# Performance work log

Hardware: AMD Instinct MI355X
Metric: run time of the kernel (lower is better)

## Reference

```python
import jax, jax.numpy as jnp
import numpy as np

HEADS = 8
DIM_HEAD = 64
QUERY_DIM = 512
CONTEXT_DIM = 512
OUT_DIM = 512
INNER = HEADS * DIM_HEAD  # 512


def setup_inputs() -> dict:
    key = jax.random.key(0)
    ks = jax.random.split(key, 6)
    B, N, S, M = 2, 1024, 4, 2048
    x = jax.random.normal(ks[0], (B, N, S, QUERY_DIM), dtype=jnp.float32)
    context = jax.random.normal(ks[1], (B, M, CONTEXT_DIM), dtype=jnp.float32)
    # Linear weights stored as [in, out] so y = x @ W (matches torch Linear with W.T)
    Wq = jax.random.normal(ks[2], (QUERY_DIM, INNER), dtype=jnp.float32) / np.sqrt(QUERY_DIM)
    Wkv = jax.random.normal(ks[3], (CONTEXT_DIM, 2 * INNER), dtype=jnp.float32) / np.sqrt(CONTEXT_DIM)
    Wo = jax.random.normal(ks[4], (INNER, OUT_DIM), dtype=jnp.float32) / np.sqrt(INNER)
    bo = jax.random.normal(ks[5], (OUT_DIM,), dtype=jnp.float32) * 0.01
    return {"x": x, "context": context, "Wq": Wq, "Wkv": Wkv, "Wo": Wo, "bo": bo}


def reference(x, context, Wq, Wkv, Wo, bo):
    B, N, S, _ = x.shape
    M = context.shape[1]
    scale = DIM_HEAD ** -0.5
    # projections
    q = (x @ Wq).reshape(B, N, S, HEADS, DIM_HEAD)            # b n s h d
    kv = context @ Wkv                                        # b m (2*inner)
    k, v = jnp.split(kv, 2, axis=-1)
    k = k.reshape(B, M, HEADS, DIM_HEAD)                      # b m h d
    v = v.reshape(B, M, HEADS, DIM_HEAD)
    # attention scores: [(b h) s n m] expressed as bhsnm
    sim = jnp.einsum('bnshd,bmhd->bhsnm', q, k) * scale
    attn = jax.nn.softmax(sim, axis=-1)
    out = jnp.einsum('bhsnm,bmhd->bnshd', attn, v)            # b n s h d
    out = out.reshape(B, N, S, INNER)
    return out @ Wo + bo
```

## Files before the change

kernel.cpp:

```cpp
#include <hip/hip_runtime.h>

typedef __bf16 bf16;
typedef __bf16 bf16x8 __attribute__((ext_vector_type(8)));
typedef __bf16 bf16x4 __attribute__((ext_vector_type(4)));
typedef float f32x4 __attribute__((ext_vector_type(4)));

#define SCL 0.18033688011112042f

#define GLOAD_LDS16(g, l)                                          \
  __builtin_amdgcn_global_load_lds(                                \
      (const __attribute__((address_space(1))) void*)(g),          \
      (__attribute__((address_space(3))) void*)(l), 16, 0, 0)

__global__ __launch_bounds__(256) void prep_kernel(const float* __restrict__ x,
                                                   const float* __restrict__ ctx,
                                                   const float* __restrict__ Wq,
                                                   const float* __restrict__ Wkv,
                                                   const float* __restrict__ Wo,
                                                   bf16* __restrict__ xb,
                                                   bf16* __restrict__ cb,
                                                   bf16* __restrict__ Wqt,
                                                   bf16* __restrict__ Wkvt,
                                                   bf16* __restrict__ Wot) {
  const int bid = blockIdx.x;
  const int tid = threadIdx.x;
  if (bid < 3072) {
    const float* src;
    bf16* dst;
    size_t off;
    if (bid < 2048) { src = x; dst = xb; off = (size_t)bid * 2048; }
    else            { src = ctx; dst = cb; off = (size_t)(bid - 2048) * 2048; }
    size_t i = off + (size_t)tid * 8;
    float4 a0 = *(const float4*)&src[i];
    float4 a1 = *(const float4*)&src[i + 4];
    bf16x8 o;
    o[0] = (bf16)a0.x; o[1] = (bf16)a0.y; o[2] = (bf16)a0.z; o[3] = (bf16)a0.w;
    o[4] = (bf16)a1.x; o[5] = (bf16)a1.y; o[6] = (bf16)a1.z; o[7] = (bf16)a1.w;
    *(bf16x8*)&dst[i] = o;
  } else {
    __shared__ float tile[32][33];
    const int idx = bid - 3072;
    const int bx = idx & 63;
    const int k0 = (idx >> 6) * 32;
    const float* W; bf16* Wt; int N, n0;
    if (bx < 16)      { W = Wq;  Wt = Wqt;  N = 512;  n0 = bx * 32; }
    else if (bx < 48) { W = Wkv; Wt = Wkvt; N = 1024; n0 = (bx - 16) * 32; }
    else              { W = Wo;  Wt = Wot;  N = 512;  n0 = (bx - 48) * 32; }
    const int j = tid & 31, i0 = tid >> 5;
#pragma unroll
    for (int ii = 0; ii < 4; ii++) {
      int i = i0 * 4 + ii;
      tile[i][j] = W[(size_t)(k0 + i) * N + n0 + j];
    }
    __syncthreads();
#pragma unroll
    for (int ii = 0; ii < 4; ii++) {
      int i = i0 * 4 + ii;
      Wt[(size_t)(n0 + i) * 512 + k0 + j] = (bf16)tile[j][i];
    }
  }
}

__device__ __forceinline__ void gemm128x64_core(const bf16* __restrict__ A,
                                                const bf16* __restrict__ Bt,
                                                int m0, int n0,
                                                bf16* As, bf16* Bs,
                                                f32x4 (&acc)[4][2],
                                                int wave, int lane) {
  const int l15 = lane & 15, quad = lane >> 4;
  const int psw = l15 & 7;
  const int lrow = lane >> 3;
  const int gchunk = (lane & 7) ^ lrow;
  const bf16* Ag = A + (size_t)(m0 + wave * 32 + lrow) * 512 + gchunk * 8;
  const bf16* Bg = Bt + (size_t)(n0 + wave * 16 + lrow) * 512 + gchunk * 8;
  bf16* Asw = As + wave * 32 * 64;
  bf16* Bsw = Bs + wave * 16 * 64;
  const int wm = (wave >> 1) * 64, wn = (wave & 1) * 32;

  for (int kt = 0; kt < 512; kt += 64) {
#pragma unroll
    for (int g = 0; g < 4; g++)
      GLOAD_LDS16(Ag + kt + (size_t)(g * 8) * 512, Asw + g * 8 * 64);
#pragma unroll
    for (int g = 0; g < 2; g++)
      GLOAD_LDS16(Bg + kt + (size_t)(g * 8) * 512, Bsw + g * 8 * 64);
    __syncthreads();
#pragma unroll
    for (int h = 0; h < 2; h++) {
      bf16x8 af[4], bfr[2];
#pragma unroll
      for (int i = 0; i < 4; i++)
        af[i] = *(const bf16x8*)&As[(wm + i * 16 + l15) * 64 + (((h * 4 + quad) ^ psw) * 8)];
#pragma unroll
      for (int j = 0; j < 2; j++)
        bfr[j] = *(const bf16x8*)&Bs[(wn + j * 16 + l15) * 64 + (((h * 4 + quad) ^ psw) * 8)];
#pragma unroll
      for (int i = 0; i < 4; i++)
#pragma unroll
        for (int j = 0; j < 2; j++)
          acc[i][j] = __builtin_amdgcn_mfma_f32_16x16x32_bf16(af[i], bfr[j], acc[i][j], 0, 0, 0);
    }
    __syncthreads();
  }
}

__global__ __launch_bounds__(256) void proj_kernel(const bf16* __restrict__ xb,
                                                   const bf16* __restrict__ cb,
                                                   const bf16* __restrict__ Wqt,
                                                   const bf16* __restrict__ Wkvt,
                                                   bf16* __restrict__ qb,
                                                   bf16* __restrict__ Kb,
                                                   bf16* __restrict__ Vtb) {
  __shared__ __align__(16) bf16 As[128 * 64];
  __shared__ __align__(16) bf16 Bs[64 * 64];
  const int tid = threadIdx.x;
  const int wave = tid >> 6, lane = tid & 63;
  const int quad = lane >> 4, l15 = lane & 15;
  const int bid = blockIdx.x;
  f32x4 acc[4][2] = {};
  const int wm = (wave >> 1) * 64, wn = (wave & 1) * 32;

  if (bid < 512) {
    const int m0 = (bid >> 3) * 128, n0 = (bid & 7) * 64;
    gemm128x64_core(xb, Wqt, m0, n0, As, Bs, acc, wave, lane);
#pragma unroll
    for (int i = 0; i < 4; i++) {
      const int rowb = m0 + wm + i * 16 + quad * 4;
#pragma unroll
      for (int j = 0; j < 2; j++) {
        const int col = n0 + wn + j * 16 + l15;
#pragma unroll
        for (int r = 0; r < 4; r++)
          qb[(size_t)(rowb + r) * 512 + col] = (bf16)(acc[i][j][r] * SCL);
      }
    }
  } else {
    const int idx = bid - 512;
    const int m0 = (idx >> 4) * 128, n0 = (idx & 15) * 64;
    gemm128x64_core(cb, Wkvt, m0, n0, As, Bs, acc, wave, lane);
#pragma unroll
    for (int i = 0; i < 4; i++) {
      const int rowb = m0 + wm + i * 16 + quad * 4;
#pragma unroll
      for (int j = 0; j < 2; j++) {
        const int col = n0 + wn + j * 16 + l15;
        if (col < 512) {
#pragma unroll
          for (int r = 0; r < 4; r++)
            Kb[(size_t)(rowb + r) * 512 + col] = (bf16)acc[i][j][r];
        } else {
          const int hh = (col - 512) >> 6, d = (col - 512) & 63;
          const int bb = rowb >> 11, mb = rowb & 2047;
          bf16x4 pk;
          pk[0] = (bf16)acc[i][j][0]; pk[1] = (bf16)acc[i][j][1];
          pk[2] = (bf16)acc[i][j][2]; pk[3] = (bf16)acc[i][j][3];
          *(bf16x4*)&Vtb[((size_t)(bb * 8 + hh) * 64 + d) * 2048 + mb] = pk;
        }
      }
    }
  }
}

__global__ __launch_bounds__(256) void outproj_kernel(const bf16* __restrict__ attn,
                                                      const bf16* __restrict__ Wot,
                                                      float* __restrict__ out,
                                                      const float* __restrict__ bias) {
  __shared__ __align__(16) bf16 As[128 * 64];
  __shared__ __align__(16) bf16 Bs[64 * 64];
  const int tid = threadIdx.x;
  const int wave = tid >> 6, lane = tid & 63;
  const int quad = lane >> 4, l15 = lane & 15;
  const int bid = blockIdx.x;
  const int m0 = (bid >> 3) * 128, n0 = (bid & 7) * 64;
  f32x4 acc[4][2] = {};
  gemm128x64_core(attn, Wot, m0, n0, As, Bs, acc, wave, lane);
  const int wm = (wave >> 1) * 64, wn = (wave & 1) * 32;
#pragma unroll
  for (int i = 0; i < 4; i++) {
    const int rowb = m0 + wm + i * 16 + quad * 4;
#pragma unroll
    for (int j = 0; j < 2; j++) {
      const int col = n0 + wn + j * 16 + l15;
      const float bv = bias[col];
#pragma unroll
      for (int r = 0; r < 4; r++)
        out[(size_t)(rowb + r) * 512 + col] = acc[i][j][r] + bv;
    }
  }
}

__global__ __launch_bounds__(256, 2) void attn_kernel(const bf16* __restrict__ q,
                                                      const bf16* __restrict__ Kb,
                                                      const bf16* __restrict__ Vtb,
                                                      bf16* __restrict__ attn_out) {
  const int tid = threadIdx.x;
  const int wave = tid >> 6, lane = tid & 63;
  const int quad = lane >> 4, l15 = lane & 15;
  const int bid = blockIdx.x;
  const int nt = bid & 7, h = (bid >> 3) & 7, s = (bid >> 6) & 3, b = bid >> 8;
  const int n0 = nt * 128;

  __shared__ __align__(16) bf16 Kl[2][64 * 64];
  __shared__ __align__(16) bf16 Vl[2][64 * 64];
  __shared__ __align__(16) bf16 Pl[4][32 * 64];
  bf16* Pw = &Pl[wave][0];

  size_t qoff[2];
  bf16x8 qf[2][2];
#pragma unroll
  for (int cg = 0; cg < 2; cg++) {
    const int n = n0 + wave * 32 + cg * 16 + l15;
    qoff[cg] = ((size_t)((b * 1024 + n) * 4 + s)) * 512 + h * 64;
    qf[cg][0] = *(const bf16x8*)&q[qoff[cg] + quad * 8];
    qf[cg][1] = *(const bf16x8*)&q[qoff[cg] + 32 + quad * 8];
  }

  f32x4 o[2][4] = {};
  f32x4 ol[2] = {};
  bf16x8 ones;
#pragma unroll
  for (int i = 0; i < 8; i++) ones[i] = (bf16)1.0f;

  const int srow = tid >> 2, c0 = tid & 3;
  const bf16* Kg = Kb + (size_t)(b * 2048 + srow) * 512 + h * 64 + c0 * 16;
  const bf16* Vg = Vtb + ((size_t)(b * 8 + h) * 64 + srow) * 2048 + c0 * 16;
  const int ssw = srow & 7;
  const int koff0 = srow * 64 + ((c0 * 2) ^ ssw) * 8;
  const int koff1 = srow * 64 + ((c0 * 2 + 1) ^ ssw) * 8;

  uint4 kr0 = *(const uint4*)Kg;
  uint4 kr1 = *(const uint4*)(Kg + 8);
  uint4 vr0 = *(const uint4*)Vg;
  uint4 vr1 = *(const uint4*)(Vg + 8);
  *(uint4*)&Kl[0][koff0] = kr0; *(uint4*)&Kl[0][koff1] = kr1;
  *(uint4*)&Vl[0][koff0] = vr0; *(uint4*)&Vl[0][koff1] = vr1;

  const int psw = l15 & 7;

  for (int t = 0; t < 32; ++t) {
    __syncthreads();
    if (t < 31) {
      const bf16* kg = Kg + (size_t)(t + 1) * 64 * 512;
      const bf16* vg = Vg + (t + 1) * 64;
      kr0 = *(const uint4*)kg; kr1 = *(const uint4*)(kg + 8);
      vr0 = *(const uint4*)vg; vr1 = *(const uint4*)(vg + 8);
    }
    const bf16* Kc = &Kl[t & 1][0];
    const bf16* Vc = &Vl[t & 1][0];

    f32x4 sf[2][4];
#pragma unroll
    for (int mc = 0; mc < 4; mc++) {
      bf16x8 kf0 = *(const bf16x8*)&Kc[(mc * 16 + l15) * 64 + ((quad ^ psw) * 8)];
      bf16x8 kf1 = *(const bf16x8*)&Kc[(mc * 16 + l15) * 64 + (((4 + quad) ^ psw) * 8)];
#pragma unroll
      for (int cg = 0; cg < 2; cg++) {
        f32x4 z = {};
        z = __builtin_amdgcn_mfma_f32_16x16x32_bf16(kf0, qf[cg][0], z, 0, 0, 0);
        z = __builtin_amdgcn_mfma_f32_16x16x32_bf16(kf1, qf[cg][1], z, 0, 0, 0);
        sf[cg][mc] = z;
      }
    }

#pragma unroll
    for (int cg = 0; cg < 2; cg++)
#pragma unroll
      for (int mc = 0; mc < 4; mc++) {
        bf16x4 pk;
        pk[0] = (bf16)__builtin_amdgcn_exp2f(sf[cg][mc][0]);
        pk[1] = (bf16)__builtin_amdgcn_exp2f(sf[cg][mc][1]);
        pk[2] = (bf16)__builtin_amdgcn_exp2f(sf[cg][mc][2]);
        pk[3] = (bf16)__builtin_amdgcn_exp2f(sf[cg][mc][3]);
        *(bf16x4*)&Pw[(cg * 16 + l15) * 64 + (((mc * 2 + (quad >> 1)) ^ psw)) * 8 + (quad & 1) * 4] = pk;
      }

#pragma unroll
    for (int mch = 0; mch < 2; mch++) {
      bf16x8 pf[2];
#pragma unroll
      for (int cg = 0; cg < 2; cg++)
        pf[cg] = *(const bf16x8*)&Pw[(cg * 16 + l15) * 64 + (((mch * 4 + quad) ^ psw)) * 8];
#pragma unroll
      for (int dg = 0; dg < 4; dg++) {
        bf16x8 vf = *(const bf16x8*)&Vc[(dg * 16 + l15) * 64 + (((mch * 4 + quad) ^ psw)) * 8];
#pragma unroll
        for (int cg = 0; cg < 2; cg++)
          o[cg][dg] = __builtin_amdgcn_mfma_f32_16x16x32_bf16(vf, pf[cg], o[cg][dg], 0, 0, 0);
      }
#pragma unroll
      for (int cg = 0; cg < 2; cg++)
        ol[cg] = __builtin_amdgcn_mfma_f32_16x16x32_bf16(ones, pf[cg], ol[cg], 0, 0, 0);
    }

    if (t < 31) {
      bf16* Kn = &Kl[(t + 1) & 1][0];
      bf16* Vn = &Vl[(t + 1) & 1][0];
      *(uint4*)&Kn[koff0] = kr0; *(uint4*)&Kn[koff1] = kr1;
      *(uint4*)&Vn[koff0] = vr0; *(uint4*)&Vn[koff1] = vr1;
    }
  }

#pragma unroll
  for (int cg = 0; cg < 2; cg++) {
    const float inv = 1.0f / ol[cg][0];
#pragma unroll
    for (int dg = 0; dg < 4; dg++) {
      bf16x4 ok;
      ok[0] = (bf16)(o[cg][dg][0] * inv); ok[1] = (bf16)(o[cg][dg][1] * inv);
      ok[2] = (bf16)(o[cg][dg][2] * inv); ok[3] = (bf16)(o[cg][dg][3] * inv);
      *(bf16x4*)&attn_out[qoff[cg] + dg * 16 + quad * 4] = ok;
    }
  }
}

extern "C" void kernel_launch(void* const* d_in, const int* in_sizes, int n_in,
                              void* d_out, int out_size, void* d_ws, size_t ws_size,
                              hipStream_t stream) {
  const float* x = (const float*)d_in[0];
  const float* context = (const float*)d_in[1];
  const float* Wq = (const float*)d_in[2];
  const float* Wkv = (const float*)d_in[3];
  const float* Wo = (const float*)d_in[4];
  const float* bo = (const float*)d_in[5];
  float* out = (float*)d_out;

  char* ws = (char*)d_ws;
  bf16* xb   = (bf16*)(ws);
  bf16* cb   = (bf16*)(ws + (8u << 20));
  bf16* qb   = (bf16*)(ws + (12u << 20));
  bf16* Kb   = (bf16*)(ws + (20u << 20));
  bf16* Vtb  = (bf16*)(ws + (24u << 20));
  bf16* Wqt  = (bf16*)(ws + (28u << 20));
  bf16* Wkvt = (bf16*)(ws + (28u << 20) + 524288);
  bf16* Wot  = (bf16*)(ws + (28u << 20) + 1572864);
  bf16* attn = xb;

  prep_kernel<<<4096, 256, 0, stream>>>(x, context, Wq, Wkv, Wo, xb, cb, Wqt, Wkvt, Wot);
  proj_kernel<<<1024, 256, 0, stream>>>(xb, cb, Wqt, Wkvt, qb, Kb, Vtb);
  attn_kernel<<<512, 256, 0, stream>>>(qb, Kb, Vtb, attn);
  outproj_kernel<<<512, 256, 0, stream>>>(attn, Wot, out, bo);
}
```

Measured before the change: 164.4 us.

## Replace LDS-staged GEMM tiles with direct register streaming and prefetch

The projection and output GEMMs no longer stage A/B tiles through shared memory with global_load_lds and barriers. Each lane now loads its MFMA operand fragments straight from global memory into registers, with a one-step register double buffer that prefetches the next k-slice. This drops LDS traffic and __syncthreads, but loses reuse across waves: each tile row is fetched by two waves, which doubles global/L2 traffic, and the per-lane strided 16-byte loads coalesce less well.

```diff
diff --git a/kernel.cpp b/kernel.cpp
--- a/kernel.cpp
+++ b/kernel.cpp
@@ -6,11 +6,6 @@
 typedef float f32x4 __attribute__((ext_vector_type(4)));
 
 #define SCL 0.18033688011112042f
-
-#define GLOAD_LDS16(g, l)                                          \
-  __builtin_amdgcn_global_load_lds(                                \
-      (const __attribute__((address_space(1))) void*)(g),          \
-      (__attribute__((address_space(3))) void*)(l), 16, 0, 0)
 
 __global__ __launch_bounds__(256) void prep_kernel(const float* __restrict__ x,
                                                    const float* __restrict__ ctx,
@@ -61,46 +56,47 @@
   }
 }
 
-__device__ __forceinline__ void gemm128x64_core(const bf16* __restrict__ A,
-                                                const bf16* __restrict__ Bt,
-                                                int m0, int n0,
-                                                bf16* As, bf16* Bs,
-                                                f32x4 (&acc)[4][2],
-                                                int wave, int lane) {
+__device__ __forceinline__ void gemm_stream_core(const bf16* __restrict__ A,
+                                                 const bf16* __restrict__ Bt,
+                                                 int m0, int n0,
+                                                 f32x4 (&acc)[4][2],
+                                                 int wave, int lane) {
   const int l15 = lane & 15, quad = lane >> 4;
-  const int psw = l15 & 7;
-  const int lrow = lane >> 3;
-  const int gchunk = (lane & 7) ^ lrow;
-  const bf16* Ag = A + (size_t)(m0 + wave * 32 + lrow) * 512 + gchunk * 8;
-  const bf16* Bg = Bt + (size_t)(n0 + wave * 16 + lrow) * 512 + gchunk * 8;
-  bf16* Asw = As + wave * 32 * 64;
-  bf16* Bsw = Bs + wave * 16 * 64;
   const int wm = (wave >> 1) * 64, wn = (wave & 1) * 32;
 
-  for (int kt = 0; kt < 512; kt += 64) {
-#pragma unroll
-    for (int g = 0; g < 4; g++)
-      GLOAD_LDS16(Ag + kt + (size_t)(g * 8) * 512, Asw + g * 8 * 64);
-#pragma unroll
-    for (int g = 0; g < 2; g++)
-      GLOAD_LDS16(Bg + kt + (size_t)(g * 8) * 512, Bsw + g * 8 * 64);
-    __syncthreads();
-#pragma unroll
-    for (int h = 0; h < 2; h++) {
-      bf16x8 af[4], bfr[2];
-#pragma unroll
-      for (int i = 0; i < 4; i++)
-        af[i] = *(const bf16x8*)&As[(wm + i * 16 + l15) * 64 + (((h * 4 + quad) ^ psw) * 8)];
+  const bf16* Ap[4];
+  const bf16* Bp[2];
+#pragma unroll
+  for (int i = 0; i < 4; i++)
+    Ap[i] = A + (size_t)(m0 + wm + i * 16 + l15) * 512 + quad * 8;
+#pragma unroll
+  for (int j = 0; j < 2; j++)
+    Bp[j] = Bt + (size_t)(n0 + wn + j * 16 + l15) * 512 + quad * 8;
+
+  bf16x8 ac[4], bc[2], an[4], bn[2];
+#pragma unroll
+  for (int i = 0; i < 4; i++) ac[i] = *(const bf16x8*)(Ap[i]);
+#pragma unroll
+  for (int j = 0; j < 2; j++) bc[j] = *(const bf16x8*)(Bp[j]);
+
+#pragma unroll
+  for (int s = 0; s < 16; s++) {
+    if (s < 15) {
+      const int off = (s + 1) * 32;
+#pragma unroll
+      for (int i = 0; i < 4; i++) an[i] = *(const bf16x8*)(Ap[i] + off);
+#pragma unroll
+      for (int j = 0; j < 2; j++) bn[j] = *(const bf16x8*)(Bp[j] + off);
+    }
+#pragma unroll
+    for (int i = 0; i < 4; i++)
 #pragma unroll
       for (int j = 0; j < 2; j++)
-        bfr[j] = *(const bf16x8*)&Bs[(wn + j * 16 + l15) * 64 + (((h * 4 + quad) ^ psw) * 8)];
-#pragma unroll
-      for (int i = 0; i < 4; i++)
-#pragma unroll
-        for (int j = 0; j < 2; j++)
-          acc[i][j] = __builtin_amdgcn_mfma_f32_16x16x32_bf16(af[i], bfr[j], acc[i][j], 0, 0, 0);
-    }
-    __syncthreads();
+        acc[i][j] = __builtin_amdgcn_mfma_f32_16x16x32_bf16(ac[i], bc[j], acc[i][j], 0, 0, 0);
+#pragma unroll
+    for (int i = 0; i < 4; i++) ac[i] = an[i];
+#pragma unroll
+    for (int j = 0; j < 2; j++) bc[j] = bn[j];
   }
 }
 
@@ -111,8 +107,6 @@
                                                    bf16* __restrict__ qb,
                                                    bf16* __restrict__ Kb,
                                                    bf16* __restrict__ Vtb) {
-  __shared__ __align__(16) bf16 As[128 * 64];
-  __shared__ __align__(16) bf16 Bs[64 * 64];
   const int tid = threadIdx.x;
   const int wave = tid >> 6, lane = tid & 63;
   const int quad = lane >> 4, l15 = lane & 15;
@@ -122,7 +116,7 @@
 
   if (bid < 512) {
     const int m0 = (bid >> 3) * 128, n0 = (bid & 7) * 64;
-    gemm128x64_core(xb, Wqt, m0, n0, As, Bs, acc, wave, lane);
+    gemm_stream_core(xb, Wqt, m0, n0, acc, wave, lane);
 #pragma unroll
     for (int i = 0; i < 4; i++) {
       const int rowb = m0 + wm + i * 16 + quad * 4;
@@ -137,7 +131,7 @@
   } else {
     const int idx = bid - 512;
     const int m0 = (idx >> 4) * 128, n0 = (idx & 15) * 64;
-    gemm128x64_core(cb, Wkvt, m0, n0, As, Bs, acc, wave, lane);
+    gemm_stream_core(cb, Wkvt, m0, n0, acc, wave, lane);
 #pragma unroll
     for (int i = 0; i < 4; i++) {
       const int rowb = m0 + wm + i * 16 + quad * 4;
@@ -165,15 +159,13 @@
                                                       const bf16* __restrict__ Wot,
                                                       float* __restrict__ out,
                                                       const float* __restrict__ bias) {
-  __shared__ __align__(16) bf16 As[128 * 64];
-  __shared__ __align__(16) bf16 Bs[64 * 64];
   const int tid = threadIdx.x;
   const int wave = tid >> 6, lane = tid & 63;
   const int quad = lane >> 4, l15 = lane & 15;
   const int bid = blockIdx.x;
   const int m0 = (bid >> 3) * 128, n0 = (bid & 7) * 64;
   f32x4 acc[4][2] = {};
-  gemm128x64_core(attn, Wot, m0, n0, As, Bs, acc, wave, lane);
+  gemm_stream_core(attn, Wot, m0, n0, acc, wave, lane);
   const int wm = (wave >> 1) * 64, wn = (wave & 1) * 32;
 #pragma unroll
   for (int i = 0; i < 4; i++) {
```

Result: slower. 206.7 us (+25.7%).

## Load V fragments directly into registers and reorder block indices for L2 reuse

Applied to the files above, without the earlier changes.

The attention kernel no longer stages V through shared memory. Each wave loads its V MFMA fragments straight from global memory into registers and double-buffers them across iterations, which removes the V LDS writes and reads and frees that LDS. Block index mapping in the projection, output-projection and attention kernels is reordered so that neighbouring blocks share the same weight columns or the same batch/head K/V, aiming for better L2 reuse. The cost is that every wave now loads the same V tile redundantly from global or L2, and the extra registers held in vcur/vnxt may hurt occupancy.

```diff
diff --git a/kernel.cpp b/kernel.cpp
--- a/kernel.cpp
+++ b/kernel.cpp
@@ -121,7 +121,7 @@
   const int wm = (wave >> 1) * 64, wn = (wave & 1) * 32;
 
   if (bid < 512) {
-    const int m0 = (bid >> 3) * 128, n0 = (bid & 7) * 64;
+    const int m0 = (bid & 63) * 128, n0 = (bid >> 6) * 64;
     gemm128x64_core(xb, Wqt, m0, n0, As, Bs, acc, wave, lane);
 #pragma unroll
     for (int i = 0; i < 4; i++) {
@@ -136,7 +136,7 @@
     }
   } else {
     const int idx = bid - 512;
-    const int m0 = (idx >> 4) * 128, n0 = (idx & 15) * 64;
+    const int m0 = (idx & 31) * 128, n0 = (idx >> 5) * 64;
     gemm128x64_core(cb, Wkvt, m0, n0, As, Bs, acc, wave, lane);
 #pragma unroll
     for (int i = 0; i < 4; i++) {
@@ -171,7 +171,7 @@
   const int wave = tid >> 6, lane = tid & 63;
   const int quad = lane >> 4, l15 = lane & 15;
   const int bid = blockIdx.x;
-  const int m0 = (bid >> 3) * 128, n0 = (bid & 7) * 64;
+  const int m0 = (bid & 63) * 128, n0 = (bid >> 6) * 64;
   f32x4 acc[4][2] = {};
   gemm128x64_core(attn, Wot, m0, n0, As, Bs, acc, wave, lane);
   const int wm = (wave >> 1) * 64, wn = (wave & 1) * 32;
@@ -197,11 +197,12 @@
   const int wave = tid >> 6, lane = tid & 63;
   const int quad = lane >> 4, l15 = lane & 15;
   const int bid = blockIdx.x;
-  const int nt = bid & 7, h = (bid >> 3) & 7, s = (bid >> 6) & 3, b = bid >> 8;
+  const int g = bid & 15, inner = bid >> 4;
+  const int b = g >> 3, h = g & 7;
+  const int s = inner & 3, nt = inner >> 2;
   const int n0 = nt * 128;
 
   __shared__ __align__(16) bf16 Kl[2][64 * 64];
-  __shared__ __align__(16) bf16 Vl[2][64 * 64];
   __shared__ __align__(16) bf16 Pl[4][32 * 64];
   bf16* Pw = &Pl[wave][0];
 
@@ -223,30 +224,39 @@
 
   const int srow = tid >> 2, c0 = tid & 3;
   const bf16* Kg = Kb + (size_t)(b * 2048 + srow) * 512 + h * 64 + c0 * 16;
-  const bf16* Vg = Vtb + ((size_t)(b * 8 + h) * 64 + srow) * 2048 + c0 * 16;
   const int ssw = srow & 7;
   const int koff0 = srow * 64 + ((c0 * 2) ^ ssw) * 8;
   const int koff1 = srow * 64 + ((c0 * 2 + 1) ^ ssw) * 8;
 
   uint4 kr0 = *(const uint4*)Kg;
   uint4 kr1 = *(const uint4*)(Kg + 8);
-  uint4 vr0 = *(const uint4*)Vg;
-  uint4 vr1 = *(const uint4*)(Vg + 8);
-  *(uint4*)&Kl[0][koff0] = kr0; *(uint4*)&Kl[0][koff1] = kr1;
-  *(uint4*)&Vl[0][koff0] = vr0; *(uint4*)&Vl[0][koff1] = vr1;
+  *(uint4*)&Kl[0][koff0] = kr0;
+  *(uint4*)&Kl[0][koff1] = kr1;
+
+  const bf16* vbase = Vtb + ((size_t)(b * 8 + h) * 64 + l15) * 2048 + quad * 8;
+
+  bf16x8 vcur[4][2], vnxt[4][2];
+#pragma unroll
+  for (int dg = 0; dg < 4; dg++)
+#pragma unroll
+    for (int mch = 0; mch < 2; mch++)
+      vcur[dg][mch] = *(const bf16x8*)(vbase + (size_t)(dg * 16) * 2048 + mch * 32);
 
   const int psw = l15 & 7;
 
   for (int t = 0; t < 32; ++t) {
     __syncthreads();
     if (t < 31) {
+#pragma unroll
+      for (int dg = 0; dg < 4; dg++)
+#pragma unroll
+        for (int mch = 0; mch < 2; mch++)
+          vnxt[dg][mch] = *(const bf16x8*)(vbase + (size_t)(dg * 16) * 2048 + (t + 1) * 64 + mch * 32);
       const bf16* kg = Kg + (size_t)(t + 1) * 64 * 512;
-      const bf16* vg = Vg + (t + 1) * 64;
-      kr0 = *(const uint4*)kg; kr1 = *(const uint4*)(kg + 8);
-      vr0 = *(const uint4*)vg; vr1 = *(const uint4*)(vg + 8);
+      kr0 = *(const uint4*)kg;
+      kr1 = *(const uint4*)(kg + 8);
     }
     const bf16* Kc = &Kl[t & 1][0];
-    const bf16* Vc = &Vl[t & 1][0];
 
     f32x4 sf[2][4];
 #pragma unroll
@@ -281,12 +291,10 @@
       for (int cg = 0; cg < 2; cg++)
         pf[cg] = *(const bf16x8*)&Pw[(cg * 16 + l15) * 64 + (((mch * 4 + quad) ^ psw)) * 8];
 #pragma unroll
-      for (int dg = 0; dg < 4; dg++) {
-        bf16x8 vf = *(const bf16x8*)&Vc[(dg * 16 + l15) * 64 + (((mch * 4 + quad) ^ psw)) * 8];
+      for (int dg = 0; dg < 4; dg++)
 #pragma unroll
         for (int cg = 0; cg < 2; cg++)
-          o[cg][dg] = __builtin_amdgcn_mfma_f32_16x16x32_bf16(vf, pf[cg], o[cg][dg], 0, 0, 0);
-      }
+          o[cg][dg] = __builtin_amdgcn_mfma_f32_16x16x32_bf16(vcur[dg][mch], pf[cg], o[cg][dg], 0, 0, 0);
 #pragma unroll
       for (int cg = 0; cg < 2; cg++)
         ol[cg] = __builtin_amdgcn_mfma_f32_16x16x32_bf16(ones, pf[cg], ol[cg], 0, 0, 0);
@@ -294,9 +302,13 @@
 
     if (t < 31) {
       bf16* Kn = &Kl[(t + 1) & 1][0];
-      bf16* Vn = &Vl[(t + 1) & 1][0];
-      *(uint4*)&Kn[koff0] = kr0; *(uint4*)&Kn[koff1] = kr1;
-      *(uint4*)&Vn[koff0] = vr0; *(uint4*)&Vn[koff1] = vr1;
+      *(uint4*)&Kn[koff0] = kr0;
+      *(uint4*)&Kn[koff1] = kr1;
+#pragma unroll
+      for (int dg = 0; dg < 4; dg++)
+#pragma unroll
+        for (int mch = 0; mch < 2; mch++)
+          vcur[dg][mch] = vnxt[dg][mch];
     }
   }
 
```

New measurement: 176.5 us. +7.4%, slower.
